# Performance work log

Measured on AMD Instinct MI355X. Metric: run time of the kernel, lower is better.

## Reference

```python
import jax, jax.numpy as jnp
import numpy as np

EPS = 1e-5

def conv1x1(x, w):
    # x: [B,C,T,D,H,W], w: [O,C] -> [B,O,T,D,H,W]
    return jnp.einsum('oc,bctdhw->botdhw', w, x)

def conv4d_3(x, w):
    # 3x3x3x3 4D conv, padding=1, stride=1, decomposed as 3 shifted 3D convs.
    # x: [B,C,T,D,H,W], w: [O,C,3,3,3,3]
    B, C, T, D, H, W = x.shape
    O = w.shape[0]
    xp = jnp.pad(x, ((0, 0), (0, 0), (1, 1), (1, 1), (1, 1), (1, 1)))
    out = None
    for k in range(3):  # small fixed loop over first kernel dim
        xk = xp[:, :, k:k + T]                      # [B,C,T,D+2,H+2,W+2]
        xk = xk.transpose(0, 2, 1, 3, 4, 5).reshape(B * T, C, D + 2, H + 2, W + 2)
        ok = jax.lax.conv_general_dilated(
            xk, w[:, :, k], window_strides=(1, 1, 1), padding='VALID',
            dimension_numbers=('NCDHW', 'OIDHW', 'NCDHW'))  # [B*T,O,D,H,W]
        out = ok if out is None else out + ok
    return out.reshape(B, T, O, D, H, W).transpose(0, 2, 1, 3, 4, 5)

def bn4d(x, g, b):
    # BatchNorm over (B, T, D, H, W) per channel (training-mode batch stats).
    axes = (0, 2, 3, 4, 5)
    m = jnp.mean(x, axis=axes, keepdims=True)
    v = jnp.mean(jnp.square(x - m), axis=axes, keepdims=True)
    sh = (1, -1, 1, 1, 1, 1)
    return (x - m) * jax.lax.rsqrt(v + EPS) * g.reshape(sh) + b.reshape(sh)

def setup_inputs() -> dict:
    key = jax.random.key(0)
    ks = jax.random.split(key, 4)
    B, C, T, D, H, W = 2, 256, 8, 16, 16, 16
    planes = 64
    return {
        'x': jax.random.normal(ks[0], (B, C, T, D, H, W), jnp.float32),
        'w1': jax.random.normal(ks[1], (planes, C), jnp.float32) * 0.05,
        'g1': jnp.ones((planes,), jnp.float32),
        'b1': jnp.zeros((planes,), jnp.float32),
        'w2': jax.random.normal(ks[2], (planes, planes, 3, 3, 3, 3), jnp.float32) * 0.05,
        'g2': jnp.ones((planes,), jnp.float32),
        'b2': jnp.zeros((planes,), jnp.float32),
        'w3': jax.random.normal(ks[3], (4 * planes, planes), jnp.float32) * 0.05,
        'g3': jnp.ones((4 * planes,), jnp.float32),
        'b3': jnp.zeros((4 * planes,), jnp.float32),
    }

def reference(x, w1, g1, b1, w2, g2, b2, w3, g3, b3):
    out = jax.nn.relu(bn4d(conv1x1(x, w1), g1, b1))
    out = jax.nn.relu(bn4d(conv4d_3(out, w2), g2, b2))
    out = bn4d(conv1x1(out, w3), g3, b3)
    return jax.nn.relu(out + x)
```

## Files before the change

kernel.cpp:

```cpp
#include <hip/hip_runtime.h>

#define S_TOT 32768

typedef unsigned short ushortT;
typedef __attribute__((ext_vector_type(8))) short short8;
typedef __attribute__((ext_vector_type(4))) float floatx4;

__device__ __forceinline__ ushortT f2bf(float f) {
    unsigned u = __float_as_uint(f);
    u = (u + 0x7fffu + ((u >> 16) & 1u)) >> 16;
    return (ushortT)u;
}
__device__ __forceinline__ float bf2f(ushortT h) {
    return __uint_as_float(((unsigned)h) << 16);
}
__device__ __forceinline__ uint32_t nrm2(uint32_t u, float a, float bs) {
    float lo = fmaxf(fmaf(a, bf2f((ushortT)(u & 0xffffu)), bs), 0.f);
    float hi = fmaxf(fmaf(a, bf2f((ushortT)(u >> 16)), bs), 0.f);
    return (uint32_t)f2bf(lo) | ((uint32_t)f2bf(hi) << 16);
}

#define NSTRIPE 8
#define STRIDE_ST 768

__global__ __launch_bounds__(256) void k_prep_w(const float* __restrict__ w1,
                                                const float* __restrict__ w2,
                                                const float* __restrict__ w3,
                                                ushortT* __restrict__ wb1,
                                                ushortT* __restrict__ wb2,
                                                ushortT* __restrict__ wb3,
                                                float* __restrict__ stats) {
    int idx = blockIdx.x * 256 + threadIdx.x;
    if (idx < 16384) {
        int e = idx;
        int j = e & 7, o = (e >> 3) & 63, q = (e >> 9) & 3, cc = e >> 11;
        int c = cc * 32 + q * 8 + j;
        wb1[e] = f2bf(w1[o * 256 + c]);
    } else if (idx < 16384 + 331776) {
        int e = idx - 16384;
        int j = e & 7, o = (e >> 3) & 63, cb = (e >> 9) & 7, tap = e >> 12;
        int c = cb * 8 + j;
        wb2[e] = f2bf(w2[((size_t)o * 64 + c) * 81 + tap]);
    } else if (idx < 16384 + 331776 + 16384) {
        int e = idx - 348160;
        int j = e & 7, o = (e >> 3) & 255, g = e >> 11;
        int ks = g >> 2, q = g & 3;
        int c = ks * 32 + q * 8 + j;
        wb3[e] = f2bf(w3[o * 64 + c]);
    } else if (idx < 364544 + NSTRIPE * STRIDE_ST) {
        stats[idx - 364544] = 0.f;
    }
}

__global__ __launch_bounds__(256) void k_coef(const float* __restrict__ stats,
                                              int off, int nch,
                                              const float* __restrict__ g,
                                              const float* __restrict__ bb,
                                              float* __restrict__ coef) {
    int c = threadIdx.x;
    if (c >= nch) return;
    float s = 0.f, qv = 0.f;
#pragma unroll
    for (int p = 0; p < NSTRIPE; ++p) {
        s  += stats[p * STRIDE_ST + off + c];
        qv += stats[p * STRIDE_ST + off + nch + c];
    }
    const float inv_n = 1.f / 65536.f;
    float mu = s * inv_n, var = qv * inv_n - mu * mu;
    float a  = g[c] * rsqrtf(var + 1e-5f);
    coef[2 * c]     = a;
    coef[2 * c + 1] = bb[c] - mu * a;
}

__global__ __launch_bounds__(256) void k_prep(const ushortT* __restrict__ yin,
                                              const float* __restrict__ coef,
                                              ushortT* __restrict__ yout) {
    size_t i = ((size_t)blockIdx.x * 256 + threadIdx.x) * 8;
    int c = (int)((i >> 15) & 63);
    float2 cf = *(const float2*)(coef + 2 * c);
    uint4 v = *(const uint4*)(yin + i);
    uint4 r;
    r.x = nrm2(v.x, cf.x, cf.y);
    r.y = nrm2(v.y, cf.x, cf.y);
    r.z = nrm2(v.z, cf.x, cf.y);
    r.w = nrm2(v.w, cf.x, cf.y);
    *(uint4*)(yout + i) = r;
}

__global__ __launch_bounds__(256) void k_conv1_mfma(const float* __restrict__ x,
                                                    const ushortT* __restrict__ wb1,
                                                    ushortT* __restrict__ y1bf,
                                                    float* __restrict__ stats) {
    __shared__ __align__(16) ushortT xb[64 * 40];

    int tid = threadIdx.x;
    int blk = blockIdx.x;
    int b  = blk >> 9;
    int n0 = (blk & 511) * 64;

    int lane = tid & 63;
    int wv   = tid >> 6;
    int m    = lane & 15;
    int q    = lane >> 4;

    int c_loc = tid & 31;
    int ng    = tid >> 5;

    floatx4 acc[4];
#pragma unroll
    for (int i = 0; i < 4; ++i) acc[i] = (floatx4){0.f, 0.f, 0.f, 0.f};

    for (int cc = 0; cc < 8; ++cc) {
        short8 afr = *(const short8*)(wb1 + (((cc * 4 + q) * 64) + wv * 16 + m) * 8);

        __syncthreads();
        {
            int c = cc * 32 + c_loc;
            const float* xp = x + ((size_t)(b * 256 + c)) * S_TOT + n0 + ng * 8;
#pragma unroll
            for (int k = 0; k < 2; ++k) {
                float4 v = *(const float4*)(xp + k * 4);
                int nb = ng * 8 + k * 4;
                xb[(nb + 0) * 40 + c_loc] = f2bf(v.x);
                xb[(nb + 1) * 40 + c_loc] = f2bf(v.y);
                xb[(nb + 2) * 40 + c_loc] = f2bf(v.z);
                xb[(nb + 3) * 40 + c_loc] = f2bf(v.w);
            }
        }
        __syncthreads();

#pragma unroll
        for (int pt = 0; pt < 4; ++pt) {
            short8 bfr = *(const short8*)(xb + (pt * 16 + m) * 40 + q * 8);
            acc[pt] = __builtin_amdgcn_mfma_f32_16x16x32_bf16(afr, bfr, acc[pt], 0, 0, 0);
        }
    }

#pragma unroll
    for (int pt = 0; pt < 4; ++pt) {
#pragma unroll
        for (int r = 0; r < 4; ++r) {
            int o = wv * 16 + q * 4 + r;
            y1bf[((size_t)(b * 64 + o)) * S_TOT + n0 + pt * 16 + m] = f2bf(acc[pt][r]);
        }
    }

    float ssum[4] = {0.f, 0.f, 0.f, 0.f}, ssq[4] = {0.f, 0.f, 0.f, 0.f};
#pragma unroll
    for (int pt = 0; pt < 4; ++pt)
#pragma unroll
        for (int r = 0; r < 4; ++r) {
            float v = acc[pt][r];
            ssum[r] += v;
            ssq[r]  += v * v;
        }
#pragma unroll
    for (int off = 1; off < 16; off <<= 1)
#pragma unroll
        for (int r = 0; r < 4; ++r) {
            ssum[r] += __shfl_xor(ssum[r], off);
            ssq[r]  += __shfl_xor(ssq[r], off);
        }
    if (m == 0) {
        float* st = stats + (blk & (NSTRIPE - 1)) * STRIDE_ST;
#pragma unroll
        for (int r = 0; r < 4; ++r) {
            int o = wv * 16 + q * 4 + r;
            atomicAdd(st + o, ssum[r]);
            atomicAdd(st + 64 + o, ssq[r]);
        }
    }
}

__global__ __launch_bounds__(256, 2) void k_conv2_mfma(
        const ushortT* __restrict__ y1n,
        const ushortT* __restrict__ wb2,
        float* __restrict__ stats,
        ushortT* __restrict__ y2bf) {
    __shared__ __align__(16) ushortT xs[108 * 64];
    __shared__ float st2[128];

    int tid = threadIdx.x;
    int blk = blockIdx.x;
    int b  = blk >> 9;
    int t  = (blk >> 6) & 7;
    int d  = (blk >> 2) & 15;
    int h0 = (blk & 3) * 4;

    int lane = tid & 63;
    int wv   = tid >> 6;
    int m    = lane & 15;
    int q    = lane >> 4;
    int wp   = wv & 1;
    int wo   = wv >> 1;

    int c2      = tid & 31;
    int prbase  = tid >> 5;

    if (tid < 128) st2[tid] = 0.f;

    const ushortT* wfb = wb2 + ((size_t)q * 64 + wo * 32 + m) * 8;

    floatx4 acc[2][2];
#pragma unroll
    for (int i = 0; i < 2; ++i)
#pragma unroll
        for (int j = 0; j < 2; ++j) acc[i][j] = (floatx4){0.f, 0.f, 0.f, 0.f};

    const size_t cstride = 32768;
    uint32_t* xsd = (uint32_t*)xs;

    for (int ktd = 0; ktd < 9; ++ktd) {
        int kt = ktd / 3, kd = ktd - kt * 3;
        int tt = t + kt - 1;
        int dd = d + kd - 1;
        bool pv = (tt >= 0 && tt < 8 && dd >= 0 && dd < 16);
        if (!pv) continue;

        __syncthreads();

        if (prbase < 6) {
            int hin = h0 + prbase - 1;
            uint32_t pack[18];
            if (hin >= 0 && hin < 16) {
                const ushortT* p0 = y1n +
                    (((size_t)(b * 64 + 2 * c2) * 8 + tt) * 16 + dd) * 256 + hin * 16;
                const ushortT* p1 = p0 + cstride;
                uint4 r0 = *(const uint4*)p0;
                uint4 r1 = *(const uint4*)(p0 + 8);
                uint4 s0v = *(const uint4*)p1;
                uint4 s1v = *(const uint4*)(p1 + 8);
                uint32_t ra[8] = {r0.x, r0.y, r0.z, r0.w, r1.x, r1.y, r1.z, r1.w};
                uint32_t sa[8] = {s0v.x, s0v.y, s0v.z, s0v.w, s1v.x, s1v.y, s1v.z, s1v.w};
                pack[0] = 0; pack[17] = 0;
#pragma unroll
                for (int k = 0; k < 8; ++k) {
                    pack[1 + 2 * k] = (ra[k] & 0xffffu) | (sa[k] << 16);
                    pack[2 + 2 * k] = (ra[k] >> 16) | (sa[k] & 0xffff0000u);
                }
            } else {
#pragma unroll
                for (int k = 0; k < 18; ++k) pack[k] = 0;
            }
            int pb = prbase * 18;
#pragma unroll
            for (int k = 0; k < 18; ++k) {
                int ppos = pb + k;
                xsd[ppos * 32 + ((((c2 >> 2) ^ (ppos & 7)) << 2) | (c2 & 3))] = pack[k];
            }
        }

        int tap0 = ktd * 9;
        short8 c00 = *(const short8*)(wfb + ((size_t)(tap0 * 8) * 64) * 8);
        short8 c01 = *(const short8*)(wfb + ((size_t)(tap0 * 8) * 64 + 16) * 8);
        short8 c10 = *(const short8*)(wfb + ((size_t)(tap0 * 8 + 4) * 64) * 8);
        short8 c11 = *(const short8*)(wfb + ((size_t)(tap0 * 8 + 4) * 64 + 16) * 8);

        __syncthreads();

#pragma unroll
        for (int khw = 0; khw < 9; ++khw) {
            short8 n00, n01, n10, n11;
            if (khw < 8) {
                int tap = tap0 + khw + 1;
                n00 = *(const short8*)(wfb + ((size_t)(tap * 8) * 64) * 8);
                n01 = *(const short8*)(wfb + ((size_t)(tap * 8) * 64 + 16) * 8);
                n10 = *(const short8*)(wfb + ((size_t)(tap * 8 + 4) * 64) * 8);
                n11 = *(const short8*)(wfb + ((size_t)(tap * 8 + 4) * 64 + 16) * 8);
            }
            int kh = khw / 3, kw = khw - kh * 3;
#pragma unroll
            for (int nt = 0; nt < 2; ++nt) {
                int ppos = (wp * 2 + nt + kh) * 18 + m + kw;
                int sw = (ppos & 7);
                const ushortT* row = xs + ppos * 64;
                short8 b0  = *(const short8*)(row + (((0 * 4 + q) ^ sw) << 3));
                short8 b1f = *(const short8*)(row + (((1 * 4 + q) ^ sw) << 3));
                acc[0][nt] = __builtin_amdgcn_mfma_f32_16x16x32_bf16(
                    c00, b0, acc[0][nt], 0, 0, 0);
                acc[1][nt] = __builtin_amdgcn_mfma_f32_16x16x32_bf16(
                    c01, b0, acc[1][nt], 0, 0, 0);
                acc[0][nt] = __builtin_amdgcn_mfma_f32_16x16x32_bf16(
                    c10, b1f, acc[0][nt], 0, 0, 0);
                acc[1][nt] = __builtin_amdgcn_mfma_f32_16x16x32_bf16(
                    c11, b1f, acc[1][nt], 0, 0, 0);
            }
            c00 = n00; c01 = n01; c10 = n10; c11 = n11;
            asm volatile("" ::: "memory");
        }
    }

#pragma unroll
    for (int ot = 0; ot < 2; ++ot) {
#pragma unroll
        for (int nt = 0; nt < 2; ++nt) {
#pragma unroll
            for (int r = 0; r < 4; ++r) {
                int o  = wo * 32 + ot * 16 + q * 4 + r;
                int hh = h0 + wp * 2 + nt;
                y2bf[(((size_t)(b * 64 + o) * 8 + t) * 16 + d) * 256 + hh * 16 + m] =
                    f2bf(acc[ot][nt][r]);
            }
        }
    }

    float ss[2][4], sqv[2][4];
#pragma unroll
    for (int ot = 0; ot < 2; ++ot)
#pragma unroll
        for (int r = 0; r < 4; ++r) {
            float s = 0.f, qv = 0.f;
#pragma unroll
            for (int nt = 0; nt < 2; ++nt) {
                float v = acc[ot][nt][r];
                s += v; qv += v * v;
            }
            ss[ot][r] = s; sqv[ot][r] = qv;
        }
#pragma unroll
    for (int off = 1; off < 16; off <<= 1)
#pragma unroll
        for (int ot = 0; ot < 2; ++ot)
#pragma unroll
            for (int r = 0; r < 4; ++r) {
                ss[ot][r]  += __shfl_xor(ss[ot][r], off);
                sqv[ot][r] += __shfl_xor(sqv[ot][r], off);
            }
    if (m == 0) {
#pragma unroll
        for (int ot = 0; ot < 2; ++ot)
#pragma unroll
            for (int r = 0; r < 4; ++r) {
                int o = wo * 32 + ot * 16 + q * 4 + r;
                atomicAdd(&st2[o], ss[ot][r]);
                atomicAdd(&st2[64 + o], sqv[ot][r]);
            }
    }
    __syncthreads();
    if (tid < 128)
        atomicAdd(stats + (blk & (NSTRIPE - 1)) * STRIDE_ST + 128 + tid, st2[tid]);
}

__global__ __launch_bounds__(256) void k_conv3_mfma(const ushortT* __restrict__ y2bf,
                                                    const ushortT* __restrict__ wb3,
                                                    const float* __restrict__ coef2,
                                                    float* __restrict__ stats,
                                                    float* __restrict__ y3) {
    __shared__ __align__(16) ushortT yb[64 * 72];

    int tid = threadIdx.x;
    int blk = blockIdx.x;
    int b  = blk >> 9;
    int n0 = (blk & 511) * 64;

    int lane = tid & 63;
    int wv   = tid >> 6;
    int m    = lane & 15;
    int q    = lane >> 4;

    for (int idx = tid; idx < 512; idx += 256) {
        int c = idx >> 3, k = idx & 7;
        float2 cc2 = *(const float2*)(coef2 + 2 * c);
        float a = cc2.x, bs = cc2.y;
        uint4 v = *(const uint4*)(y2bf + ((size_t)(b * 64 + c)) * S_TOT + n0 + k * 8);
        uint32_t va[4] = {v.x, v.y, v.z, v.w};
#pragma unroll
        for (int p = 0; p < 4; ++p) {
            float lo = fmaxf(fmaf(a, bf2f((ushortT)(va[p] & 0xffffu)), bs), 0.f);
            float hi = fmaxf(fmaf(a, bf2f((ushortT)(va[p] >> 16)), bs), 0.f);
            yb[(k * 8 + 2 * p)     * 72 + c] = f2bf(lo);
            yb[(k * 8 + 2 * p + 1) * 72 + c] = f2bf(hi);
        }
    }
    __syncthreads();

    floatx4 acc[4][4];
#pragma unroll
    for (int i = 0; i < 4; ++i)
#pragma unroll
        for (int j = 0; j < 4; ++j) acc[i][j] = (floatx4){0.f, 0.f, 0.f, 0.f};

#pragma unroll
    for (int ks = 0; ks < 2; ++ks) {
        short8 afr[4];
#pragma unroll
        for (int ot = 0; ot < 4; ++ot)
            afr[ot] = *(const short8*)(wb3 +
                (((ks * 4 + q) * 256) + wv * 64 + ot * 16 + m) * 8);
#pragma unroll
        for (int pt = 0; pt < 4; ++pt) {
            short8 bfr = *(const short8*)(yb + (pt * 16 + m) * 72 + ks * 32 + q * 8);
#pragma unroll
            for (int ot = 0; ot < 4; ++ot)
                acc[ot][pt] = __builtin_amdgcn_mfma_f32_16x16x32_bf16(
                    afr[ot], bfr, acc[ot][pt], 0, 0, 0);
        }
    }

#pragma unroll
    for (int ot = 0; ot < 4; ++ot) {
#pragma unroll
        for (int pt = 0; pt < 4; ++pt) {
#pragma unroll
            for (int r = 0; r < 4; ++r) {
                int o = wv * 64 + ot * 16 + q * 4 + r;
                y3[((size_t)(b * 256 + o)) * S_TOT + n0 + pt * 16 + m] = acc[ot][pt][r];
            }
        }
    }

    float ssum[4][4], ssq[4][4];
#pragma unroll
    for (int ot = 0; ot < 4; ++ot)
#pragma unroll
        for (int r = 0; r < 4; ++r) {
            float s = 0.f, qv = 0.f;
#pragma unroll
            for (int pt = 0; pt < 4; ++pt) {
                float v = acc[ot][pt][r];
                s += v; qv += v * v;
            }
            ssum[ot][r] = s; ssq[ot][r] = qv;
        }
#pragma unroll
    for (int off = 1; off < 16; off <<= 1)
#pragma unroll
        for (int ot = 0; ot < 4; ++ot)
#pragma unroll
            for (int r = 0; r < 4; ++r) {
                ssum[ot][r] += __shfl_xor(ssum[ot][r], off);
                ssq[ot][r]  += __shfl_xor(ssq[ot][r], off);
            }
    if (m == 0) {
        float* st = stats + (blk & (NSTRIPE - 1)) * STRIDE_ST;
#pragma unroll
        for (int ot = 0; ot < 4; ++ot)
#pragma unroll
            for (int r = 0; r < 4; ++r) {
                int o = wv * 64 + ot * 16 + q * 4 + r;
                atomicAdd(st + 256 + o, ssum[ot][r]);
                atomicAdd(st + 512 + o, ssq[ot][r]);
            }
    }
}

__global__ __launch_bounds__(256) void k_final(const float* __restrict__ x,
                                               const float* __restrict__ stats,
                                               const float* __restrict__ g,
                                               const float* __restrict__ bb,
                                               float* __restrict__ out) {
    size_t i = ((size_t)blockIdx.x * 256 + threadIdx.x) * 4;
    int o = (int)((blockIdx.x >> 5) & 255);
    float s = 0.f, qv = 0.f;
#pragma unroll
    for (int p = 0; p < NSTRIPE; ++p) {
        s  += stats[p * STRIDE_ST + 256 + o];
        qv += stats[p * STRIDE_ST + 512 + o];
    }
    const float n = 65536.f;
    float mean = s / n;
    float var  = qv / n - mean * mean;
    float a  = g[o] * rsqrtf(var + 1e-5f);
    float bs = bb[o] - mean * a;
    float4 y  = *(float4*)(out + i);
    float4 xv = *(const float4*)(x + i);
    float4 r;
    r.x = fmaxf(a * y.x + bs + xv.x, 0.f);
    r.y = fmaxf(a * y.y + bs + xv.y, 0.f);
    r.z = fmaxf(a * y.z + bs + xv.z, 0.f);
    r.w = fmaxf(a * y.w + bs + xv.w, 0.f);
    *(float4*)(out + i) = r;
}

extern "C" void kernel_launch(void* const* d_in, const int* in_sizes, int n_in,
                              void* d_out, int out_size, void* d_ws, size_t ws_size,
                              hipStream_t stream) {
    const float* x  = (const float*)d_in[0];
    const float* w1 = (const float*)d_in[1];
    const float* g1 = (const float*)d_in[2];
    const float* b1 = (const float*)d_in[3];
    const float* w2 = (const float*)d_in[4];
    const float* g2 = (const float*)d_in[5];
    const float* b2 = (const float*)d_in[6];
    const float* w3 = (const float*)d_in[7];
    const float* g3 = (const float*)d_in[8];
    const float* b3 = (const float*)d_in[9];

    char* ws = (char*)d_ws;
    ushortT* y1bf = (ushortT*)(ws);
    ushortT* y1n  = (ushortT*)(ws + 8388608);
    ushortT* y2bf = (ushortT*)(ws + 16777216);
    ushortT* wb1  = (ushortT*)(ws + 25165824);
    ushortT* wb2  = (ushortT*)(ws + 25198592);
    ushortT* wb3  = (ushortT*)(ws + 25862144);
    float*   stats = (float*)(ws + 25894912);
    float*   coef1 = (float*)(ws + 25919488);
    float*   coef2 = (float*)(ws + 25920000);
    float* y3 = (float*)d_out;

    k_prep_w     <<<1448,  256, 0, stream>>>(w1, w2, w3, wb1, wb2, wb3, stats);
    k_conv1_mfma <<<1024,  256, 0, stream>>>(x, wb1, y1bf, stats);
    k_coef       <<<1,     256, 0, stream>>>(stats, 0, 64, g1, b1, coef1);
    k_prep       <<<2048,  256, 0, stream>>>(y1bf, coef1, y1n);
    k_conv2_mfma <<<1024,  256, 0, stream>>>(y1n, wb2, stats, y2bf);
    k_coef       <<<1,     256, 0, stream>>>(stats, 128, 64, g2, b2, coef2);
    k_conv3_mfma <<<1024,  256, 0, stream>>>(y2bf, wb3, coef2, stats, y3);
    k_final      <<<16384, 256, 0, stream>>>(x, stats, g3, b3, y3);
}
```

Measured before the change: 253.4 us.

## Double-buffer LDS tile in conv1 MFMA kernel to overlap loads with compute

Adds a second LDS buffer in the first 1x1 conv kernel. The global loads of x and the weights for the next 32-channel chunk are issued before the MFMAs on the current chunk, and the converted tile is written into the other buffer afterwards. This hides global load latency behind the matrix ops and drops one barrier per iteration, at the cost of doubling LDS use and holding more registers for the prefetched values.

```diff
diff --git a/kernel.cpp b/kernel.cpp
--- a/kernel.cpp
+++ b/kernel.cpp
@@ -91,7 +91,7 @@
                                                     const ushortT* __restrict__ wb1,
                                                     ushortT* __restrict__ y1bf,
                                                     float* __restrict__ stats) {
-    __shared__ __align__(16) ushortT xb[64 * 40];
+    __shared__ __align__(16) ushortT xb[2][64 * 40];
 
     int tid = threadIdx.x;
     int blk = blockIdx.x;
@@ -106,34 +106,60 @@
     int c_loc = tid & 31;
     int ng    = tid >> 5;
 
+    const float* xbase = x + ((size_t)(b * 256 + c_loc)) * S_TOT + n0 + ng * 8;
+
     floatx4 acc[4];
 #pragma unroll
     for (int i = 0; i < 4; ++i) acc[i] = (floatx4){0.f, 0.f, 0.f, 0.f};
 
+    short8 afr = *(const short8*)(wb1 + ((q * 64) + wv * 16 + m) * 8);
+    {
+        float4 v0 = *(const float4*)(xbase);
+        float4 v1 = *(const float4*)(xbase + 4);
+        int nb = ng * 8;
+        ushortT* xd = xb[0];
+        xd[(nb + 0) * 40 + c_loc] = f2bf(v0.x);
+        xd[(nb + 1) * 40 + c_loc] = f2bf(v0.y);
+        xd[(nb + 2) * 40 + c_loc] = f2bf(v0.z);
+        xd[(nb + 3) * 40 + c_loc] = f2bf(v0.w);
+        xd[(nb + 4) * 40 + c_loc] = f2bf(v1.x);
+        xd[(nb + 5) * 40 + c_loc] = f2bf(v1.y);
+        xd[(nb + 6) * 40 + c_loc] = f2bf(v1.z);
+        xd[(nb + 7) * 40 + c_loc] = f2bf(v1.w);
+    }
+    __syncthreads();
+
     for (int cc = 0; cc < 8; ++cc) {
-        short8 afr = *(const short8*)(wb1 + (((cc * 4 + q) * 64) + wv * 16 + m) * 8);
-
+        short8 nafr;
+        float4 n0v, n1v;
+        if (cc < 7) {
+            nafr = *(const short8*)(wb1 + ((((cc + 1) * 4 + q) * 64) + wv * 16 + m) * 8);
+            const float* xp = xbase + (size_t)(cc + 1) * 32 * S_TOT;
+            n0v = *(const float4*)(xp);
+            n1v = *(const float4*)(xp + 4);
+        }
+
+        const ushortT* xc = xb[cc & 1];
+#pragma unroll
+        for (int pt = 0; pt < 4; ++pt) {
+            short8 bfr = *(const short8*)(xc + (pt * 16 + m) * 40 + q * 8);
+            acc[pt] = __builtin_amdgcn_mfma_f32_16x16x32_bf16(afr, bfr, acc[pt], 0, 0, 0);
+        }
+
+        if (cc < 7) {
+            int nb = ng * 8;
+            ushortT* xd = xb[(cc + 1) & 1];
+            xd[(nb + 0) * 40 + c_loc] = f2bf(n0v.x);
+            xd[(nb + 1) * 40 + c_loc] = f2bf(n0v.y);
+            xd[(nb + 2) * 40 + c_loc] = f2bf(n0v.z);
+            xd[(nb + 3) * 40 + c_loc] = f2bf(n0v.w);
+            xd[(nb + 4) * 40 + c_loc] = f2bf(n1v.x);
+            xd[(nb + 5) * 40 + c_loc] = f2bf(n1v.y);
+            xd[(nb + 6) * 40 + c_loc] = f2bf(n1v.z);
+            xd[(nb + 7) * 40 + c_loc] = f2bf(n1v.w);
+            afr = nafr;
+        }
         __syncthreads();
-        {
-            int c = cc * 32 + c_loc;
-            const float* xp = x + ((size_t)(b * 256 + c)) * S_TOT + n0 + ng * 8;
-#pragma unroll
-            for (int k = 0; k < 2; ++k) {
-                float4 v = *(const float4*)(xp + k * 4);
-                int nb = ng * 8 + k * 4;
-                xb[(nb + 0) * 40 + c_loc] = f2bf(v.x);
-                xb[(nb + 1) * 40 + c_loc] = f2bf(v.y);
-                xb[(nb + 2) * 40 + c_loc] = f2bf(v.z);
-                xb[(nb + 3) * 40 + c_loc] = f2bf(v.w);
-            }
-        }
-        __syncthreads();
-
-#pragma unroll
-        for (int pt = 0; pt < 4; ++pt) {
-            short8 bfr = *(const short8*)(xb + (pt * 16 + m) * 40 + q * 8);
-            acc[pt] = __builtin_amdgcn_mfma_f32_16x16x32_bf16(afr, bfr, acc[pt], 0, 0, 0);
-        }
     }
 
 #pragma unroll
```

Measured after the change: 255.1 us. Within noise of the previous version (+0.7%).
